# Optimization experiments

Measured on AMD Instinct MI355X. Metric: run time of the kernel, lower is better.

The kernel has to match this reference:

```python
import jax, jax.numpy as jnp
import numpy as np

N_NODES = 100000
DROPOUT_P = 0.2


def _gcn_conv(x, W, b, src, dst, n_nodes):
    # PyG GCNConv: h = x @ W; add self-loops; sym-norm deg^-1/2 aggregation; + bias
    h = x @ W  # [N, D_out]
    loops = jnp.arange(n_nodes, dtype=src.dtype)
    src_all = jnp.concatenate([src, loops])
    dst_all = jnp.concatenate([dst, loops])
    deg = jax.ops.segment_sum(jnp.ones_like(dst_all, dtype=h.dtype), dst_all,
                              num_segments=n_nodes)  # includes self-loops
    dinv = jnp.where(deg > 0, jax.lax.rsqrt(deg), 0.0)
    norm = dinv[src_all] * dinv[dst_all]  # [E+N]
    msg = h[src_all] * norm[:, None]      # gather + scale
    out = jax.ops.segment_sum(msg, dst_all, num_segments=n_nodes)  # scatter-add
    return out + b


def setup_inputs() -> dict:
    key = jax.random.key(0)
    k1, k2, k3, k4 = jax.random.split(key, 4)
    x = jax.random.normal(k1, (N_NODES, 128), dtype=jnp.float32)
    edge_index = jax.random.randint(k2, (2, 1600000), 0, N_NODES, dtype=jnp.int64)
    W1 = jax.random.normal(k3, (128, 64), dtype=jnp.float32) * (1.0 / np.sqrt(128))
    b1 = jnp.zeros((64,), dtype=jnp.float32)
    W2 = jax.random.normal(k4, (64, 32), dtype=jnp.float32) * (1.0 / np.sqrt(64))
    b2 = jnp.zeros((32,), dtype=jnp.float32)
    return {"x": x, "edge_index": edge_index, "W1": W1, "b1": b1, "W2": W2, "b2": b2}


def reference(x, edge_index, W1, b1, W2, b2):
    src, dst = edge_index[0], edge_index[1]
    h1 = _gcn_conv(x, W1, b1, src, dst, N_NODES)
    h1 = jax.nn.relu(h1)
    # F.dropout defaults to training=True -> apply inverted dropout with fixed key
    keep = jax.random.bernoulli(jax.random.key(42), 1.0 - DROPOUT_P, h1.shape)
    h1 = jnp.where(keep, h1 / (1.0 - DROPOUT_P), 0.0)
    h2 = _gcn_conv(h1, W2, b2, src, dst, N_NODES)
    return h2
```

## Files before the change

### kernel.cpp

```cpp
#include <hip/hip_runtime.h>
#include <stdint.h>

#define DIN 128
#define D1 64
#define D2 32
#define MAXDEG 48
#define BCAP 4608
#define CBLK 8192

__device__ __forceinline__ unsigned short f2bf(float v) {
  unsigned u = __float_as_uint(v);
  unsigned r = u + 0x7fffu + ((u >> 16) & 1u);
  return (unsigned short)(r >> 16);
}
__device__ __forceinline__ float bflo(unsigned u) { return __uint_as_float(u << 16); }
__device__ __forceinline__ float bfhi(unsigned u) { return __uint_as_float(u & 0xffff0000u); }

__device__ __forceinline__ unsigned rotl32(unsigned x, int r) {
  return (x << r) | (x >> (32 - r));
}

__device__ __forceinline__ unsigned threefry_fold(unsigned ctr) {
  unsigned k0 = 0u, k1 = 42u;
  unsigned ks0 = k0, ks1 = k1, ks2 = k0 ^ k1 ^ 0x1BD11BDAu;
  unsigned x0 = 0u, x1 = ctr;
  x0 += ks0; x1 += ks1;
#define TF_ROUND(r) { x0 += x1; x1 = rotl32(x1, (r)); x1 ^= x0; }
  TF_ROUND(13) TF_ROUND(15) TF_ROUND(26) TF_ROUND(6)
  x0 += ks1; x1 += ks2 + 1u;
  TF_ROUND(17) TF_ROUND(29) TF_ROUND(16) TF_ROUND(24)
  x0 += ks2; x1 += ks0 + 2u;
  TF_ROUND(13) TF_ROUND(15) TF_ROUND(26) TF_ROUND(6)
  x0 += ks0; x1 += ks1 + 3u;
  TF_ROUND(17) TF_ROUND(29) TF_ROUND(16) TF_ROUND(24)
  x0 += ks1; x1 += ks2 + 4u;
  TF_ROUND(13) TF_ROUND(15) TF_ROUND(26) TF_ROUND(6)
  x0 += ks2; x1 += ks0 + 5u;
#undef TF_ROUND
  return x0 ^ x1;
}

__device__ __forceinline__ float dropout_scale(unsigned idx) {
  unsigned bits = threefry_fold(idx);
  float u = __uint_as_float((bits >> 9) | 0x3f800000u) - 1.0f;
  return (u < 0.8f) ? 1.25f : 0.0f;
}

__device__ __forceinline__ uint4 grow64(const unsigned short* p, int s, int fc) {
  return *(const uint4*)((const char*)p + (((unsigned)s << 7) + ((unsigned)fc << 1)));
}
__device__ __forceinline__ uint4 grow32(const unsigned short* p, int s, int fc) {
  return *(const uint4*)((const char*)p + (((unsigned)s << 6) + ((unsigned)fc << 1)));
}

__device__ __forceinline__ void addpk(float2& a, unsigned u) {
  a.x += bflo(u);
  a.y += bfhi(u);
}
__device__ __forceinline__ void addpkm(float2& a, unsigned u, float m) {
  a.x = fmaf(m, bflo(u), a.x);
  a.y = fmaf(m, bfhi(u), a.y);
}

__global__ __launch_bounds__(256) void bin_kernel(const int* __restrict__ src,
                                                  const int* __restrict__ dst,
                                                  int* __restrict__ cursor,
                                                  uint2* __restrict__ binned,
                                                  int E, int NBK) {
  __shared__ int cnt[512];
  __shared__ int cbase[512];
  const int tid = threadIdx.x;
  const int e0 = blockIdx.x * CBLK;

  for (int b = tid; b < NBK; b += 256) cnt[b] = 0;
  __syncthreads();

#pragma unroll 4
  for (int i = 0; i < CBLK / 256; i++) {
    int e = e0 + tid + 256 * i;
    if (e < E) atomicAdd(&cnt[dst[e] >> 8], 1);
  }
  __syncthreads();

  for (int b = tid; b < NBK; b += 256) {
    int c = cnt[b];
    if (c > 0) cbase[b] = b * BCAP + atomicAdd(&cursor[b], c);
    cnt[b] = 0;
  }
  __syncthreads();

#pragma unroll 4
  for (int i = 0; i < CBLK / 256; i++) {
    int e = e0 + tid + 256 * i;
    if (e < E) {
      int d = dst[e];
      int b = d >> 8;
      int rk = atomicAdd(&cnt[b], 1);
      int pos = cbase[b] + rk;
      if (pos - b * BCAP < BCAP)
        binned[pos] = make_uint2((unsigned)d, (unsigned)src[e]);
    }
  }
}

__global__ __launch_bounds__(256) void ellbuild_kernel(const uint2* __restrict__ binned,
                                                       const int* __restrict__ cursor,
                                                       int* __restrict__ deg,
                                                       float* __restrict__ dinv,
                                                       int* __restrict__ ell, int N) {
  __shared__ int r[256];
  const int tid = threadIdx.x;
  const int b = blockIdx.x;
  const int nodebase = b << 8;
  r[tid] = 0;
  __syncthreads();

  int cnt = cursor[b];
  if (cnt > BCAP) cnt = BCAP;
  const uint2* seg = binned + (size_t)b * BCAP;
  for (int i = tid; i < cnt; i += 256) {
    uint2 p = seg[i];
    int local = (int)p.x - nodebase;
    int rk = atomicAdd(&r[local], 1);
    if (rk < MAXDEG) ell[(int)p.x * MAXDEG + rk] = (int)p.y;
  }
  __syncthreads();

  int node = nodebase + tid;
  if (node < N) {
    int dg = r[tid];
    deg[node] = dg;
    dinv[node] = (float)(1.0 / sqrt((double)(dg + 1)));
  }
}

__global__ __launch_bounds__(256) void gemm1_kernel(const float* __restrict__ x,
                                                    const float* __restrict__ W1,
                                                    const float* __restrict__ dinv,
                                                    unsigned short* __restrict__ h1p, int N) {
  __shared__ float xT[32][65];
  __shared__ float Wl[32][D1];
  const int tid = threadIdx.x;
  const int rowbase = blockIdx.x * 64;
  const int tx = tid & 15;
  const int ty = tid >> 4;
  float acc[4][4];
#pragma unroll
  for (int i = 0; i < 4; i++)
#pragma unroll
    for (int j = 0; j < 4; j++) acc[i][j] = 0.f;

  for (int c4 = 0; c4 < 4; c4++) {
    const int k0 = c4 * 32;
#pragma unroll
    for (int i = 0; i < 2; i++) {
      int f = tid + 256 * i;
      int row = f >> 3;
      int kq = (f & 7) * 4;
      int gr = rowbase + row;
      float4 vv = make_float4(0.f, 0.f, 0.f, 0.f);
      if (gr < N) vv = *(const float4*)(x + (size_t)gr * DIN + k0 + kq);
      xT[kq + 0][row] = vv.x;
      xT[kq + 1][row] = vv.y;
      xT[kq + 2][row] = vv.z;
      xT[kq + 3][row] = vv.w;
    }
#pragma unroll
    for (int i = 0; i < 2; i++) {
      int f = tid + 256 * i;
      int k = f >> 4;
      int cc = (f & 15) * 4;
      *(float4*)&Wl[k][cc] = *(const float4*)(W1 + (size_t)(k0 + k) * D1 + cc);
    }
    __syncthreads();
#pragma unroll 4
    for (int k = 0; k < 32; k++) {
      float4 a = *(const float4*)&xT[k][4 * ty];
      float4 b = *(const float4*)&Wl[k][4 * tx];
      float av[4] = {a.x, a.y, a.z, a.w};
      float bv[4] = {b.x, b.y, b.z, b.w};
#pragma unroll
      for (int i = 0; i < 4; i++)
#pragma unroll
        for (int j = 0; j < 4; j++) acc[i][j] = fmaf(av[i], bv[j], acc[i][j]);
    }
    __syncthreads();
  }

#pragma unroll
  for (int i = 0; i < 4; i++) {
    int gr = rowbase + 4 * ty + i;
    if (gr < N) {
      float di = dinv[gr];
      ushort4 o;
      o.x = f2bf(acc[i][0] * di);
      o.y = f2bf(acc[i][1] * di);
      o.z = f2bf(acc[i][2] * di);
      o.w = f2bf(acc[i][3] * di);
      *(ushort4*)(h1p + (size_t)gr * D1 + 4 * tx) = o;
    }
  }
}

__global__ __launch_bounds__(256) void agg1_kernel(const int* __restrict__ deg,
                                                   const float* __restrict__ dinv,
                                                   const int* __restrict__ ell,
                                                   const unsigned short* __restrict__ h1p,
                                                   const float* __restrict__ b1,
                                                   float* __restrict__ h1d, int N) {
  __shared__ float red[4][512];
  const int wslot = __builtin_amdgcn_readfirstlane(threadIdx.x >> 6);
  const int d = blockIdx.x * 4 + wslot;
  const int lane = threadIdx.x & 63;
  const int eslot = lane >> 3;
  const int fc = (lane & 7) << 3;
  const int cnt = min(deg[d], MAXDEG);
  const int base = d * MAXDEG;

  float2 acc[4];
  {
    uint4 sv = grow64(h1p, d, fc);
    float m = (eslot == 0) ? 1.0f : 0.0f;
    acc[0] = make_float2(m * bflo(sv.x), m * bfhi(sv.x));
    acc[1] = make_float2(m * bflo(sv.y), m * bfhi(sv.y));
    acc[2] = make_float2(m * bflo(sv.z), m * bfhi(sv.z));
    acc[3] = make_float2(m * bflo(sv.w), m * bfhi(sv.w));
  }

  int j = 0;
  for (; j + 16 <= cnt; j += 16) {
    int s0 = ell[base + j + eslot];
    int s1 = ell[base + j + 8 + eslot];
    uint4 v0 = grow64(h1p, s0, fc);
    uint4 v1 = grow64(h1p, s1, fc);
    addpk(acc[0], v0.x); addpk(acc[1], v0.y); addpk(acc[2], v0.z); addpk(acc[3], v0.w);
    addpk(acc[0], v1.x); addpk(acc[1], v1.y); addpk(acc[2], v1.z); addpk(acc[3], v1.w);
  }
  if (j < cnt) {
    int e0 = j + eslot;
    int e1 = e0 + 8;
    int s0 = ell[base + e0];
    int s1 = ell[base + e1];
    s0 = (e0 < cnt) ? s0 : d;
    s1 = (e1 < cnt) ? s1 : d;
    float m0 = (e0 < cnt) ? 1.0f : 0.0f;
    float m1 = (e1 < cnt) ? 1.0f : 0.0f;
    uint4 v0 = grow64(h1p, s0, fc);
    uint4 v1 = grow64(h1p, s1, fc);
    addpkm(acc[0], v0.x, m0); addpkm(acc[1], v0.y, m0); addpkm(acc[2], v0.z, m0); addpkm(acc[3], v0.w, m0);
    addpkm(acc[0], v1.x, m1); addpkm(acc[1], v1.y, m1); addpkm(acc[2], v1.z, m1); addpkm(acc[3], v1.w, m1);
  }

  float* wred = red[wslot];
  *(float4*)&wred[eslot * 64 + fc]     = make_float4(acc[0].x, acc[0].y, acc[1].x, acc[1].y);
  *(float4*)&wred[eslot * 64 + fc + 4] = make_float4(acc[2].x, acc[2].y, acc[3].x, acc[3].y);
  const int f = fc + eslot;
  float v = 0.f;
#pragma unroll
  for (int e = 0; e < 8; e++) v += wred[e * 64 + f];

  float o = fmaf(dinv[d], v, b1[f]);
  o = fmaxf(o, 0.0f);
  o *= dropout_scale((unsigned)(d * D1 + f));
  h1d[(size_t)d * D1 + f] = o;
}

__global__ __launch_bounds__(256) void gemm2_kernel(const float* __restrict__ h1d,
                                                    const float* __restrict__ W2,
                                                    const float* __restrict__ dinv,
                                                    unsigned short* __restrict__ h2p, int N) {
  __shared__ float hT[D1][129];
  __shared__ float Wl[D1][D2];
  const int tid = threadIdx.x;
  const int rowbase = blockIdx.x * 128;

#pragma unroll
  for (int i = 0; i < 8; i++) {
    int f = tid + 256 * i;
    int row = f >> 4;
    int kq = (f & 15) * 4;
    int gr = rowbase + row;
    float4 v = make_float4(0.f, 0.f, 0.f, 0.f);
    if (gr < N) v = *(const float4*)(h1d + (size_t)gr * D1 + kq);
    hT[kq + 0][row] = v.x;
    hT[kq + 1][row] = v.y;
    hT[kq + 2][row] = v.z;
    hT[kq + 3][row] = v.w;
  }
#pragma unroll
  for (int i = 0; i < 2; i++) {
    int f = tid + 256 * i;
    int k = f >> 3;
    int c = (f & 7) * 4;
    *(float4*)&Wl[k][c] = *(const float4*)(W2 + (size_t)k * D2 + c);
  }
  __syncthreads();

  const int tx = tid & 7;
  const int ty = tid >> 3;
  float acc[4][4];
#pragma unroll
  for (int i = 0; i < 4; i++)
#pragma unroll
    for (int j = 0; j < 4; j++) acc[i][j] = 0.f;

#pragma unroll 4
  for (int k = 0; k < D1; k++) {
    float4 a = *(const float4*)&hT[k][4 * ty];
    float4 b = *(const float4*)&Wl[k][4 * tx];
    float av[4] = {a.x, a.y, a.z, a.w};
    float bv[4] = {b.x, b.y, b.z, b.w};
#pragma unroll
    for (int i = 0; i < 4; i++)
#pragma unroll
      for (int j = 0; j < 4; j++) acc[i][j] = fmaf(av[i], bv[j], acc[i][j]);
  }

#pragma unroll
  for (int i = 0; i < 4; i++) {
    int gr = rowbase + 4 * ty + i;
    if (gr < N) {
      float di = dinv[gr];
      ushort4 o;
      o.x = f2bf(acc[i][0] * di);
      o.y = f2bf(acc[i][1] * di);
      o.z = f2bf(acc[i][2] * di);
      o.w = f2bf(acc[i][3] * di);
      *(ushort4*)(h2p + (size_t)gr * D2 + 4 * tx) = o;
    }
  }
}

__global__ __launch_bounds__(256) void agg2_kernel(const int* __restrict__ deg,
                                                   const float* __restrict__ dinv,
                                                   const int* __restrict__ ell,
                                                   const unsigned short* __restrict__ h2p,
                                                   const float* __restrict__ b2,
                                                   float* __restrict__ out, int N) {
  __shared__ float red[4][512];
  const int wslot = __builtin_amdgcn_readfirstlane(threadIdx.x >> 6);
  const int d = blockIdx.x * 4 + wslot;
  const int lane = threadIdx.x & 63;
  const int eslot = lane >> 2;
  const int fc = (lane & 3) << 3;
  const int cnt = min(deg[d], MAXDEG);
  const int base = d * MAXDEG;

  float2 acc[4];
  {
    uint4 sv = grow32(h2p, d, fc);
    float m = (eslot == 0) ? 1.0f : 0.0f;
    acc[0] = make_float2(m * bflo(sv.x), m * bfhi(sv.x));
    acc[1] = make_float2(m * bflo(sv.y), m * bfhi(sv.y));
    acc[2] = make_float2(m * bflo(sv.z), m * bfhi(sv.z));
    acc[3] = make_float2(m * bflo(sv.w), m * bfhi(sv.w));
  }

  int j = 0;
  for (; j + 16 <= cnt; j += 16) {
    int s = ell[base + j + eslot];
    uint4 v = grow32(h2p, s, fc);
    addpk(acc[0], v.x); addpk(acc[1], v.y); addpk(acc[2], v.z); addpk(acc[3], v.w);
  }
  if (j < cnt) {
    int e = j + eslot;
    int s = ell[base + e];
    s = (e < cnt) ? s : d;
    float m = (e < cnt) ? 1.0f : 0.0f;
    uint4 v = grow32(h2p, s, fc);
    addpkm(acc[0], v.x, m); addpkm(acc[1], v.y, m); addpkm(acc[2], v.z, m); addpkm(acc[3], v.w, m);
  }

  float* wred = red[wslot];
  *(float4*)&wred[eslot * 32 + fc]     = make_float4(acc[0].x, acc[0].y, acc[1].x, acc[1].y);
  *(float4*)&wred[eslot * 32 + fc + 4] = make_float4(acc[2].x, acc[2].y, acc[3].x, acc[3].y);
  const int f = fc + (eslot & 7);
  const int ebase = (lane >= 32) ? 8 : 0;
  float v = 0.f;
#pragma unroll
  for (int e = 0; e < 8; e++) v += wred[(ebase + e) * 32 + f];
  v += __shfl_down(v, 32, 64);

  if (lane < 32) {
    out[(size_t)d * D2 + f] = fmaf(dinv[d], v, b2[f]);
  }
}

extern "C" void kernel_launch(void* const* d_in, const int* in_sizes, int n_in,
                              void* d_out, int out_size, void* d_ws, size_t ws_size,
                              hipStream_t stream) {
  const float* x  = (const float*)d_in[0];
  const int*   ei = (const int*)d_in[1];
  const float* W1 = (const float*)d_in[2];
  const float* b1 = (const float*)d_in[3];
  const float* W2 = (const float*)d_in[4];
  const float* b2 = (const float*)d_in[5];
  const int N = in_sizes[0] / DIN;
  const int E = in_sizes[1] / 2;
  const int NBK = (N + 255) >> 8;
  const int* src = ei;
  const int* dst = ei + E;
  float* out = (float*)d_out;

  char* ws = (char*)d_ws;
  size_t off = 0;
  auto alloc = [&](size_t bytes) -> char* {
    char* p = ws + off;
    off += (bytes + 255) / 256 * 256;
    return p;
  };
  unsigned short* h1p = (unsigned short*)alloc((size_t)N * D1 * 2);
  float*          h1d = (float*)alloc((size_t)N * D1 * 4);
  int*            ell = (int*)alloc(((size_t)N * MAXDEG + 64) * 4);
  int*            deg = (int*)alloc((size_t)N * 4);
  float*        dinvp = (float*)alloc((size_t)N * 4);
  int*         cursor = (int*)alloc((size_t)NBK * 4);
  unsigned short* h2p = h1p;
  uint2*       binned = (uint2*)h1d;
  (void)ws_size; (void)n_in; (void)out_size;

  hipMemsetAsync(cursor, 0, (size_t)NBK * 4, stream);

  bin_kernel<<<(E + CBLK - 1) / CBLK, 256, 0, stream>>>(src, dst, cursor, binned, E, NBK);
  ellbuild_kernel<<<NBK, 256, 0, stream>>>(binned, cursor, deg, dinvp, ell, N);
  gemm1_kernel<<<(N + 63) / 64, 256, 0, stream>>>(x, W1, dinvp, h1p, N);
  agg1_kernel<<<N / 4, 256, 0, stream>>>(deg, dinvp, ell, h1p, b1, h1d, N);
  gemm2_kernel<<<(N + 127) / 128, 256, 0, stream>>>(h1d, W2, dinvp, h2p, N);
  agg2_kernel<<<N / 4, 256, 0, stream>>>(deg, dinvp, ell, h2p, b2, out, N);
}
```

Baseline: 255.4 us.

## Build ELL adjacency with direct global atomics and pad LDS reduction rows

Replaces the two-pass binned ELL construction (LDS-histogram binning followed by per-bucket ELL build) with one scatter kernel that does a global atomicAdd on each destination's degree and writes the source directly into its ELL slot. A small separate kernel then computes the degree-based normalisation. The aim is to cut a full pass over the edge list, the intermediate binned buffer and the cursor memset. The cost is more contended global atomics and fully random ELL writes with less locality. It also pads the per-wave LDS reduction rows in both aggregation kernels (stride 66/34) to reduce bank conflicts, though this makes odd rows of the float4 stores only 8-byte aligned.

```diff
diff --git a/kernel.cpp b/kernel.cpp
--- a/kernel.cpp
+++ b/kernel.cpp
@@ -5,8 +5,6 @@
 #define D1 64
 #define D2 32
 #define MAXDEG 48
-#define BCAP 4608
-#define CBLK 8192
 
 __device__ __forceinline__ unsigned short f2bf(float v) {
   unsigned u = __float_as_uint(v);
@@ -62,76 +60,22 @@
   a.y = fmaf(m, bfhi(u), a.y);
 }
 
-__global__ __launch_bounds__(256) void bin_kernel(const int* __restrict__ src,
-                                                  const int* __restrict__ dst,
-                                                  int* __restrict__ cursor,
-                                                  uint2* __restrict__ binned,
-                                                  int E, int NBK) {
-  __shared__ int cnt[512];
-  __shared__ int cbase[512];
-  const int tid = threadIdx.x;
-  const int e0 = blockIdx.x * CBLK;
-
-  for (int b = tid; b < NBK; b += 256) cnt[b] = 0;
-  __syncthreads();
-
-#pragma unroll 4
-  for (int i = 0; i < CBLK / 256; i++) {
-    int e = e0 + tid + 256 * i;
-    if (e < E) atomicAdd(&cnt[dst[e] >> 8], 1);
-  }
-  __syncthreads();
-
-  for (int b = tid; b < NBK; b += 256) {
-    int c = cnt[b];
-    if (c > 0) cbase[b] = b * BCAP + atomicAdd(&cursor[b], c);
-    cnt[b] = 0;
-  }
-  __syncthreads();
-
-#pragma unroll 4
-  for (int i = 0; i < CBLK / 256; i++) {
-    int e = e0 + tid + 256 * i;
-    if (e < E) {
-      int d = dst[e];
-      int b = d >> 8;
-      int rk = atomicAdd(&cnt[b], 1);
-      int pos = cbase[b] + rk;
-      if (pos - b * BCAP < BCAP)
-        binned[pos] = make_uint2((unsigned)d, (unsigned)src[e]);
-    }
-  }
-}
-
-__global__ __launch_bounds__(256) void ellbuild_kernel(const uint2* __restrict__ binned,
-                                                       const int* __restrict__ cursor,
-                                                       int* __restrict__ deg,
-                                                       float* __restrict__ dinv,
-                                                       int* __restrict__ ell, int N) {
-  __shared__ int r[256];
-  const int tid = threadIdx.x;
-  const int b = blockIdx.x;
-  const int nodebase = b << 8;
-  r[tid] = 0;
-  __syncthreads();
-
-  int cnt = cursor[b];
-  if (cnt > BCAP) cnt = BCAP;
-  const uint2* seg = binned + (size_t)b * BCAP;
-  for (int i = tid; i < cnt; i += 256) {
-    uint2 p = seg[i];
-    int local = (int)p.x - nodebase;
-    int rk = atomicAdd(&r[local], 1);
-    if (rk < MAXDEG) ell[(int)p.x * MAXDEG + rk] = (int)p.y;
-  }
-  __syncthreads();
-
-  int node = nodebase + tid;
-  if (node < N) {
-    int dg = r[tid];
-    deg[node] = dg;
-    dinv[node] = (float)(1.0 / sqrt((double)(dg + 1)));
-  }
+__global__ __launch_bounds__(256) void scatter_kernel(const int* __restrict__ src,
+                                                      const int* __restrict__ dst,
+                                                      int* __restrict__ deg,
+                                                      int* __restrict__ ell, int E) {
+  int e = blockIdx.x * 256 + threadIdx.x;
+  if (e >= E) return;
+  int d = dst[e];
+  int s = src[e];
+  int rk = atomicAdd(&deg[d], 1);
+  if (rk < MAXDEG) ell[d * MAXDEG + rk] = s;
+}
+
+__global__ __launch_bounds__(256) void dinv_kernel(const int* __restrict__ deg,
+                                                   float* __restrict__ dinv, int N) {
+  int i = blockIdx.x * 256 + threadIdx.x;
+  if (i < N) dinv[i] = (float)(1.0 / sqrt((double)(deg[i] + 1)));
 }
 
 __global__ __launch_bounds__(256) void gemm1_kernel(const float* __restrict__ x,
@@ -208,7 +152,7 @@
                                                    const unsigned short* __restrict__ h1p,
                                                    const float* __restrict__ b1,
                                                    float* __restrict__ h1d, int N) {
-  __shared__ float red[4][512];
+  __shared__ float red[4][528];
   const int wslot = __builtin_amdgcn_readfirstlane(threadIdx.x >> 6);
   const int d = blockIdx.x * 4 + wslot;
   const int lane = threadIdx.x & 63;
@@ -252,12 +196,12 @@
   }
 
   float* wred = red[wslot];
-  *(float4*)&wred[eslot * 64 + fc]     = make_float4(acc[0].x, acc[0].y, acc[1].x, acc[1].y);
-  *(float4*)&wred[eslot * 64 + fc + 4] = make_float4(acc[2].x, acc[2].y, acc[3].x, acc[3].y);
+  *(float4*)&wred[eslot * 66 + fc]     = make_float4(acc[0].x, acc[0].y, acc[1].x, acc[1].y);
+  *(float4*)&wred[eslot * 66 + fc + 4] = make_float4(acc[2].x, acc[2].y, acc[3].x, acc[3].y);
   const int f = fc + eslot;
   float v = 0.f;
 #pragma unroll
-  for (int e = 0; e < 8; e++) v += wred[e * 64 + f];
+  for (int e = 0; e < 8; e++) v += wred[e * 66 + f];
 
   float o = fmaf(dinv[d], v, b1[f]);
   o = fmaxf(o, 0.0f);
@@ -337,7 +281,7 @@
                                                    const unsigned short* __restrict__ h2p,
                                                    const float* __restrict__ b2,
                                                    float* __restrict__ out, int N) {
-  __shared__ float red[4][512];
+  __shared__ float red[4][544];
   const int wslot = __builtin_amdgcn_readfirstlane(threadIdx.x >> 6);
   const int d = blockIdx.x * 4 + wslot;
   const int lane = threadIdx.x & 63;
@@ -372,13 +316,13 @@
   }
 
   float* wred = red[wslot];
-  *(float4*)&wred[eslot * 32 + fc]     = make_float4(acc[0].x, acc[0].y, acc[1].x, acc[1].y);
-  *(float4*)&wred[eslot * 32 + fc + 4] = make_float4(acc[2].x, acc[2].y, acc[3].x, acc[3].y);
+  *(float4*)&wred[eslot * 34 + fc]     = make_float4(acc[0].x, acc[0].y, acc[1].x, acc[1].y);
+  *(float4*)&wred[eslot * 34 + fc + 4] = make_float4(acc[2].x, acc[2].y, acc[3].x, acc[3].y);
   const int f = fc + (eslot & 7);
   const int ebase = (lane >= 32) ? 8 : 0;
   float v = 0.f;
 #pragma unroll
-  for (int e = 0; e < 8; e++) v += wred[(ebase + e) * 32 + f];
+  for (int e = 0; e < 8; e++) v += wred[(ebase + e) * 34 + f];
   v += __shfl_down(v, 32, 64);
 
   if (lane < 32) {
@@ -397,7 +341,6 @@
   const float* b2 = (const float*)d_in[5];
   const int N = in_sizes[0] / DIN;
   const int E = in_sizes[1] / 2;
-  const int NBK = (N + 255) >> 8;
   const int* src = ei;
   const int* dst = ei + E;
   float* out = (float*)d_out;
@@ -414,15 +357,13 @@
   int*            ell = (int*)alloc(((size_t)N * MAXDEG + 64) * 4);
   int*            deg = (int*)alloc((size_t)N * 4);
   float*        dinvp = (float*)alloc((size_t)N * 4);
-  int*         cursor = (int*)alloc((size_t)NBK * 4);
   unsigned short* h2p = h1p;
-  uint2*       binned = (uint2*)h1d;
   (void)ws_size; (void)n_in; (void)out_size;
 
-  hipMemsetAsync(cursor, 0, (size_t)NBK * 4, stream);
-
-  bin_kernel<<<(E + CBLK - 1) / CBLK, 256, 0, stream>>>(src, dst, cursor, binned, E, NBK);
-  ellbuild_kernel<<<NBK, 256, 0, stream>>>(binned, cursor, deg, dinvp, ell, N);
+  hipMemsetAsync(deg, 0, (size_t)N * 4, stream);
+
+  scatter_kernel<<<(E + 255) / 256, 256, 0, stream>>>(src, dst, deg, ell, E);
+  dinv_kernel<<<(N + 255) / 256, 256, 0, stream>>>(deg, dinvp, N);
   gemm1_kernel<<<(N + 63) / 64, 256, 0, stream>>>(x, W1, dinvp, h1p, N);
   agg1_kernel<<<N / 4, 256, 0, stream>>>(deg, dinvp, ell, h1p, b1, h1d, N);
   gemm2_kernel<<<(N + 127) / 128, 256, 0, stream>>>(h1d, W2, dinvp, h2p, N);
```

Measured after the change: 340.5 us. +33.3%, slower.
